# Performance work log

Hardware: AMD Instinct MI355X
Metric: run time of the kernel (lower is better)

Reference implementation:

```python
import jax, jax.numpy as jnp
import numpy as np

B, T, H, P, N = 32, 512, 128, 16, 16
D = 4 * H


def _lstm(x, Wih, Whh, bih, bhh):
    # standard torch-style LSTM, batch_first input x: [B, T, 1], zero init state
    Bz = x.shape[0]
    Hh = Whh.shape[1]
    h0 = jnp.zeros((Bz, Hh), x.dtype)

    def step(carry, xt):
        h, c = carry
        g = xt @ Wih.T + bih + h @ Whh.T + bhh  # [B, 4H], gate order i,f,g,o
        i, f, gg, o = jnp.split(g, 4, axis=-1)
        c = jax.nn.sigmoid(f) * c + jax.nn.sigmoid(i) * jnp.tanh(gg)
        h = jax.nn.sigmoid(o) * jnp.tanh(c)
        return (h, c), h

    _, hs = jax.lax.scan(step, (h0, h0), jnp.swapaxes(x, 0, 1))
    return jnp.swapaxes(hs, 0, 1)  # [B, T, H]


def _forward(Y, Xp, Xn, Xi, init_c, init_h, Wih, Whh, bih, bhh,
             Wc, Uc, bc, Wg, Ug, bg, Wf, Uf, bf, Wo, Uo, bo, Wa,
             Watt, batt, vatt, W1, b1, W2, b2, W3, b3):
    run = lambda x: _lstm(x, Wih, Whh, bih, bhh)
    Y1 = run(Y)                                              # [B,T,H]
    Xi1 = run(Xi)
    Xp1 = jnp.mean(jax.vmap(run)(jnp.moveaxis(Xp, 1, 0)), axis=0)  # mean over P stocks
    Xn1 = jnp.mean(jax.vmap(run)(jnp.moveaxis(Xn, 1, 0)), axis=0)
    result = jnp.concatenate([Y1, Xp1, Xn1, Xi1], axis=2)    # [B,T,4H]

    Hh = Wa.shape[0]

    def mi_step(carry, xt):  # Mi-LSTM cell: 4 input streams with gated-candidate attention
        c, h = carry
        xs = xt.reshape(xt.shape[0], 4, Hh)                  # split 4H into 4 streams
        cand = jnp.tanh(jnp.einsum('bkh,khj->bkj', xs, Wc) + jnp.einsum('bh,khj->bkj', h, Uc) + bc)
        ig = jax.nn.sigmoid(jnp.einsum('bkh,khj->bkj', xs, Wg) + jnp.einsum('bh,khj->bkj', h, Ug) + bg)
        l = ig * cand                                        # [B,4,H]
        a = jax.nn.softmax(jnp.einsum('bkj,bj->bk', l, c @ Wa), axis=1)
        lmix = jnp.einsum('bk,bkj->bj', a, l)
        f = jax.nn.sigmoid(xt @ Wf + h @ Uf + bf)
        o = jax.nn.sigmoid(xt @ Wo + h @ Uo + bo)
        c = f * c + lmix
        h = o * jnp.tanh(c)
        return (c, h), h

    _, hs = jax.lax.scan(mi_step, (init_c, init_h), jnp.swapaxes(result, 0, 1))
    Y2 = jnp.swapaxes(hs, 0, 1)                              # [B,T,H]

    # temporal attention over the Mi-LSTM outputs
    scores = jnp.tanh(Y2 @ Watt + batt) @ vatt               # [B,T]
    attw = jax.nn.softmax(scores, axis=1)
    Y3 = jnp.einsum('bt,bth->bh', attw, Y2)                  # [B,H]

    hm = jax.nn.relu(Y3 @ W1 + b1)
    hm = jax.nn.relu(hm @ W2 + b2)
    return hm @ W3 + b3                                      # [B,1]


def setup_inputs() -> dict:
    key = jax.random.key(0)
    ks = jax.random.split(key, 24)
    u = lambda k, s: jax.random.uniform(k, s, dtype=jnp.float32)
    nr = lambda k, s: jax.random.normal(k, s, dtype=jnp.float32) * 0.05
    z = lambda s: jnp.zeros(s, jnp.float32)
    return {
        'Y': u(ks[0], (B, T, 1)), 'Xp': u(ks[1], (B, P, T, 1)), 'Xn': u(ks[2], (B, N, T, 1)),
        'Xi': u(ks[3], (B, T, 1)), 'Target': u(ks[4], (B, 1)),
        'init_c': u(ks[5], (B, H)), 'init_h': u(ks[6], (B, H)),
        'Wih': nr(ks[7], (4 * H, 1)), 'Whh': nr(ks[8], (4 * H, H)), 'bih': z(4 * H), 'bhh': z(4 * H),
        'Wc': nr(ks[9], (4, H, H)), 'Uc': nr(ks[10], (4, H, H)), 'bc': z((4, H)),
        'Wg': nr(ks[11], (4, H, H)), 'Ug': nr(ks[12], (4, H, H)), 'bg': z((4, H)),
        'Wf': nr(ks[13], (D, H)), 'Uf': nr(ks[14], (H, H)), 'bf': z(H),
        'Wo': nr(ks[15], (D, H)), 'Uo': nr(ks[16], (H, H)), 'bo': z(H),
        'Wa': nr(ks[17], (H, H)),
        'Watt': nr(ks[18], (H, H)), 'batt': z(H), 'vatt': nr(ks[19], (H,)),
        'W1': nr(ks[20], (H, H)), 'b1': z(H),
        'W2': nr(ks[21], (H, H)), 'b2': z(H),
        'W3': nr(ks[22], (H, 1)), 'b3': z(1),
    }


def reference(Y, Xp, Xn, Xi, Target, init_c, init_h, Wih, Whh, bih, bhh,
              Wc, Uc, bc, Wg, Ug, bg, Wf, Uf, bf, Wo, Uo, bo, Wa,
              Watt, batt, vatt, W1, b1, W2, b2, W3, b3):
    out = _forward(Y, Xp, Xn, Xi, init_c, init_h, Wih, Whh, bih, bhh,
                   Wc, Uc, bc, Wg, Ug, bg, Wf, Uf, bf, Wo, Uo, bo, Wa,
                   Watt, batt, vatt, W1, b1, W2, b2, W3, b3)
    loss = jnp.mean((out - Target) ** 2)
    return out, loss
```

## Files before the change

### kernel.cpp

```cpp
#include <hip/hip_runtime.h>
#include <hip/hip_fp16.h>

typedef _Float16 half8 __attribute__((ext_vector_type(8)));
typedef float float4_ __attribute__((ext_vector_type(4)));

__device__ __forceinline__ float rcp_(float x) { return __builtin_amdgcn_rcpf(x); }
__device__ __forceinline__ float sigf(float x) { return rcp_(1.f + __expf(-x)); }
__device__ __forceinline__ float tanhf2(float x) {
  x = fminf(fmaxf(x, -15.f), 15.f);
  float e = __expf(-2.f * x);
  return (1.f - e) * rcp_(1.f + e);
}

__global__ __launch_bounds__(512, 2)
void k1_lstm(const float* __restrict__ Y, const float* __restrict__ Xp,
             const float* __restrict__ Xn, const float* __restrict__ Xi,
             const float* __restrict__ Wih, const float* __restrict__ Whh,
             const float* __restrict__ bih, const float* __restrict__ bhh,
             _Float16* __restrict__ result)
{
  __shared__ float x_lds[16][513];
  __shared__ _Float16 hbuf[2][16][136];

  const int tid  = threadIdx.x;
  const int wv   = tid >> 6;
  const int lane = tid & 63;
  const int cl   = lane & 15;
  const int rowg = lane >> 4;
  const int bid  = blockIdx.x;

  const float* xsrc; int slot; int do_mean; int b_out_base;
  if (bid < 2)       { xsrc = Y  + (size_t)(bid * 16) * 512;        slot = 0; do_mean = 0; b_out_base = bid * 16; }
  else if (bid < 4)  { xsrc = Xi + (size_t)((bid - 2) * 16) * 512;  slot = 3; do_mean = 0; b_out_base = (bid - 2) * 16; }
  else if (bid < 36) { xsrc = Xp + (size_t)((bid - 4) * 16) * 512;  slot = 1; do_mean = 1; b_out_base = bid - 4; }
  else               { xsrc = Xn + (size_t)((bid - 36) * 16) * 512; slot = 2; do_mean = 1; b_out_base = bid - 36; }

  for (int i = tid; i < 16 * 512; i += 512) {
    int r = i >> 9, t = i & 511;
    x_lds[r][t] = xsrc[r * 512 + t];
  }
  for (int i = tid; i < 16 * 136; i += 512) {
    hbuf[0][i / 136][i % 136] = (_Float16)0.f;
  }

  const int cg = wv * 16 + cl;
  half8 bw[4][4];
  #pragma unroll
  for (int g = 0; g < 4; ++g) {
    #pragma unroll
    for (int kc = 0; kc < 4; ++kc) {
      const float* p = Whh + (size_t)(g * 128 + cg) * 128 + kc * 32 + rowg * 8;
      half8 v;
      #pragma unroll
      for (int j = 0; j < 8; ++j) v[j] = (_Float16)p[j];
      bw[g][kc] = v;
    }
  }
  float wih_r[4], bias_r[4];
  #pragma unroll
  for (int g = 0; g < 4; ++g) {
    wih_r[g]  = Wih[g * 128 + cg];
    bias_r[g] = bih[g * 128 + cg] + bhh[g * 128 + cg];
  }

  float c_reg[4] = {0.f, 0.f, 0.f, 0.f};
  float hvp[4] = {0.f, 0.f, 0.f, 0.f};
  float sprev = 0.f;
  __syncthreads();

  for (int t = 0; t < 512; ++t) {
    if (t > 0) {
      if (!do_mean) {
        #pragma unroll
        for (int i = 0; i < 4; ++i) {
          int b = b_out_base + rowg * 4 + i;
          result[(((size_t)b * 512 + (t - 1)) * 4 + slot) * 128 + cg] = (_Float16)hvp[i];
        }
      } else {
        if (rowg == 0)
          result[(((size_t)b_out_base * 512 + (t - 1)) * 4 + slot) * 128 + cg] = (_Float16)sprev;
      }
    }

    const int cur = t & 1;
    half8 a[4];
    #pragma unroll
    for (int kc = 0; kc < 4; ++kc)
      a[kc] = *(const half8*)&hbuf[cur][cl][kc * 32 + rowg * 8];

    float4_ acc[4];
    #pragma unroll
    for (int g = 0; g < 4; ++g) {
      float4_ z = {0.f, 0.f, 0.f, 0.f};
      #pragma unroll
      for (int kc = 0; kc < 4; ++kc)
        z = __builtin_amdgcn_mfma_f32_16x16x32_f16(a[kc], bw[g][kc], z, 0, 0, 0);
      acc[g] = z;
    }

    float hv[4];
    #pragma unroll
    for (int i = 0; i < 4; ++i) {
      const int row = rowg * 4 + i;
      float x  = x_lds[row][t];
      float ui = acc[0][i] + x * wih_r[0] + bias_r[0];
      float uf = acc[1][i] + x * wih_r[1] + bias_r[1];
      float ug = acc[2][i] + x * wih_r[2] + bias_r[2];
      float uo = acc[3][i] + x * wih_r[3] + bias_r[3];
      float ii = sigf(ui), ff = sigf(uf), gg = tanhf2(ug), oo = sigf(uo);
      float c  = ff * c_reg[i] + ii * gg;
      c_reg[i] = c;
      float h  = oo * tanhf2(c);
      hv[i] = h;
      hbuf[cur ^ 1][row][cg] = (_Float16)h;
    }

    if (!do_mean) {
      #pragma unroll
      for (int i = 0; i < 4; ++i) hvp[i] = hv[i];
    } else {
      float s = hv[0] + hv[1] + hv[2] + hv[3];
      s += __shfl_xor(s, 16, 64);
      s += __shfl_xor(s, 32, 64);
      sprev = s * 0.0625f;
    }
    __syncthreads();
  }

  if (!do_mean) {
    #pragma unroll
    for (int i = 0; i < 4; ++i) {
      int b = b_out_base + rowg * 4 + i;
      result[(((size_t)b * 512 + 511) * 4 + slot) * 128 + cg] = (_Float16)hvp[i];
    }
  } else {
    if (rowg == 0)
      result[(((size_t)b_out_base * 512 + 511) * 4 + slot) * 128 + cg] = (_Float16)sprev;
  }
}

__global__ __launch_bounds__(512, 2)
void k2_gemm(const _Float16* __restrict__ result,
             const float* __restrict__ Wc, const float* __restrict__ Wg,
             const float* __restrict__ Wf, const float* __restrict__ Wo,
             _Float16* __restrict__ candX, _Float16* __restrict__ igX,
             _Float16* __restrict__ fX, _Float16* __restrict__ oX)
{
  __shared__ _Float16 a_lds[128][136];
  __shared__ _Float16 bt_lds[256][136];

  const int tid   = threadIdx.x;
  const int lane  = tid & 63;
  const int wv    = tid >> 6;
  const int cl    = lane & 15, rowg = lane >> 4;
  const int mtile = blockIdx.x;
  const int role  = blockIdx.y;

  const int nchunks = (role == 0) ? 4 : 1;
  const int kstream = role - 1;

  float4_ acc[16];
  #pragma unroll
  for (int n = 0; n < 16; ++n) acc[n] = (float4_){0.f, 0.f, 0.f, 0.f};

  for (int ch = 0; ch < nchunks; ++ch) {
    const int koff = (role == 0) ? ch * 128 : kstream * 128;
    for (int i = tid; i < 1024; i += 512) {
      int r = i >> 3, v8 = i & 7;
      half8 val = *(const half8*)&result[((size_t)(mtile * 128 + r)) * 512 + koff + v8 * 8];
      *(half8*)&a_lds[r][v8 * 8] = val;
    }
    for (int i = tid; i < 128 * 256; i += 512) {
      int n = i & 255, kk = i >> 8;
      float w;
      if (role == 0) {
        w = (n < 128) ? Wf[(size_t)(ch * 128 + kk) * 128 + n]
                      : Wo[(size_t)(ch * 128 + kk) * 128 + (n - 128)];
      } else {
        w = (n < 128) ? Wc[(size_t)(kstream * 128 + kk) * 128 + n]
                      : Wg[(size_t)(kstream * 128 + kk) * 128 + (n - 128)];
      }
      bt_lds[n][kk] = (_Float16)w;
    }
    __syncthreads();
    #pragma unroll
    for (int kc = 0; kc < 4; ++kc) {
      half8 a = *(const half8*)&a_lds[wv * 16 + cl][kc * 32 + rowg * 8];
      #pragma unroll
      for (int n = 0; n < 16; ++n) {
        half8 bb = *(const half8*)&bt_lds[n * 16 + cl][kc * 32 + rowg * 8];
        acc[n] = __builtin_amdgcn_mfma_f32_16x16x32_f16(a, bb, acc[n], 0, 0, 0);
      }
    }
    __syncthreads();
  }

  #pragma unroll
  for (int n = 0; n < 16; ++n) {
    int col = n * 16 + cl;
    #pragma unroll
    for (int i = 0; i < 4; ++i) {
      size_t r = (size_t)mtile * 128 + wv * 16 + rowg * 4 + i;
      _Float16 v = (_Float16)acc[n][i];
      if (role == 0) {
        if (col < 128) fX[r * 128 + col] = v;
        else           oX[r * 128 + (col - 128)] = v;
      } else {
        if (col < 128) candX[(r * 4 + kstream) * 128 + col] = v;
        else           igX  [(r * 4 + kstream) * 128 + (col - 128)] = v;
      }
    }
  }
}

__global__ __launch_bounds__(512, 1)
void k3_scan(const float* __restrict__ Uc, const float* __restrict__ Ug,
             const float* __restrict__ Uf, const float* __restrict__ Uo,
             const float* __restrict__ Wa,
             const float* __restrict__ bc, const float* __restrict__ bg,
             const float* __restrict__ bfv, const float* __restrict__ bov,
             const float* __restrict__ init_c, const float* __restrict__ init_h,
             const _Float16* __restrict__ candX, const _Float16* __restrict__ igX,
             const _Float16* __restrict__ fX, const _Float16* __restrict__ oX,
             _Float16* __restrict__ Y2)
{
  __shared__ __align__(16) unsigned h_pk[64];
  __shared__ __align__(16) unsigned c_pk[64];
  __shared__ float c_f32[128];
  __shared__ __align__(16) float raw[1408];
  __shared__ float part2[2][4];

  const int tid  = threadIdx.x;
  const int b    = blockIdx.x;
  const int wv   = tid >> 6;
  const int lane = tid & 63;
  const int cl   = lane & 15;
  const int rowg = lane >> 4;

  half8 wfrag[11][4];
  #pragma unroll
  for (int gi = 0; gi < 11; ++gi) {
    const int col = (wv * 11 + gi) * 16 + cl;
    const float* src;
    if (col < 512)       src = Uc + (col >> 7) * 16384 + (col & 127);
    else if (col < 1024) src = Ug + ((col >> 7) - 4) * 16384 + (col & 127);
    else if (col < 1152) src = Uf + (col - 1024);
    else if (col < 1280) src = Uo + (col - 1152);
    else                 src = Wa + (col - 1280);
    #pragma unroll
    for (int kc = 0; kc < 4; ++kc) {
      half8 v;
      #pragma unroll
      for (int j = 0; j < 8; ++j)
        v[j] = (_Float16)src[(kc * 32 + rowg * 8 + j) * 128];
      wfrag[gi][kc] = v;
    }
  }

  float bc_r[4] = {0, 0, 0, 0}, bg_r[4] = {0, 0, 0, 0}, bf_r = 0.f, bo_r = 0.f;
  if (tid < 128) {
    #pragma unroll
    for (int k = 0; k < 4; ++k) { bc_r[k] = bc[k * 128 + tid]; bg_r[k] = bg[k * 128 + tid]; }
    bf_r = bfv[tid]; bo_r = bov[tid];
    c_f32[tid] = init_c[b * 128 + tid];
  }
  if (tid < 64) {
    union { _Float16 h[2]; unsigned u; } hp, cp;
    hp.h[0] = (_Float16)init_h[b * 128 + 2 * tid];
    hp.h[1] = (_Float16)init_h[b * 128 + 2 * tid + 1];
    cp.h[0] = (_Float16)init_c[b * 128 + 2 * tid];
    cp.h[1] = (_Float16)init_c[b * 128 + 2 * tid + 1];
    h_pk[tid] = hp.u;
    c_pk[tid] = cp.u;
  }
  __syncthreads();

  float hprev = 0.f;

  for (int t = 0; t < 512; ++t) {
    if (t > 0 && tid < 128)
      Y2[((size_t)b * 512 + (t - 1)) * 128 + tid] = (_Float16)hprev;

    float cx[4] = {0, 0, 0, 0}, gx[4] = {0, 0, 0, 0}, fx = 0.f, ox = 0.f;
    if (tid < 128) {
      size_t r = (size_t)b * 512 + t;
      #pragma unroll
      for (int k = 0; k < 4; ++k) {
        cx[k] = (float)candX[(r * 4 + k) * 128 + tid];
        gx[k] = (float)igX  [(r * 4 + k) * 128 + tid];
      }
      fx = (float)fX[r * 128 + tid];
      ox = (float)oX[r * 128 + tid];
    }

    {
      const uint4* hp4 = (const uint4*)h_pk;
      const uint4* cp4 = (const uint4*)c_pk;
      union { uint4 u; half8 h; } hb[4], cb[4];
      #pragma unroll
      for (int kc = 0; kc < 4; ++kc) {
        hb[kc].u = hp4[kc * 4 + rowg];
        cb[kc].u = cp4[kc * 4 + rowg];
      }
      #pragma unroll
      for (int gi = 0; gi < 11; ++gi) {
        const int g = wv * 11 + gi;
        float4_ acc = {0.f, 0.f, 0.f, 0.f};
        if (g < 80) {
          #pragma unroll
          for (int kc = 0; kc < 4; ++kc)
            acc = __builtin_amdgcn_mfma_f32_16x16x32_f16(wfrag[gi][kc], hb[kc].h, acc, 0, 0, 0);
        } else {
          #pragma unroll
          for (int kc = 0; kc < 4; ++kc)
            acc = __builtin_amdgcn_mfma_f32_16x16x32_f16(wfrag[gi][kc], cb[kc].h, acc, 0, 0, 0);
        }
        if (cl == 0)
          *(float4_*)&raw[g * 16 + rowg * 4] = acc;
      }
    }
    __syncthreads();

    float l0 = 0.f, l1 = 0.f, l2 = 0.f, l3 = 0.f, fj = 0.f, oj = 0.f;
    if (tid < 128) {
      float cand[4], ig[4];
      #pragma unroll
      for (int k = 0; k < 4; ++k) {
        float uc = cx[k] + raw[k * 128 + tid] + bc_r[k];
        float ui = gx[k] + raw[512 + k * 128 + tid] + bg_r[k];
        cand[k] = tanhf2(uc);
        ig[k]   = sigf(ui);
      }
      l0 = ig[0] * cand[0]; l1 = ig[1] * cand[1];
      l2 = ig[2] * cand[2]; l3 = ig[3] * cand[3];
      float cwa = raw[1280 + tid];
      float p0 = l0 * cwa, p1 = l1 * cwa, p2 = l2 * cwa, p3 = l3 * cwa;
      #pragma unroll
      for (int m = 1; m < 64; m <<= 1) {
        p0 += __shfl_xor(p0, m, 64);
        p1 += __shfl_xor(p1, m, 64);
        p2 += __shfl_xor(p2, m, 64);
        p3 += __shfl_xor(p3, m, 64);
      }
      if ((tid & 63) == 0) {
        part2[tid >> 6][0] = p0; part2[tid >> 6][1] = p1;
        part2[tid >> 6][2] = p2; part2[tid >> 6][3] = p3;
      }
      fj = sigf(fx + raw[1024 + tid] + bf_r);
      oj = sigf(ox + raw[1152 + tid] + bo_r);
    }
    __syncthreads();

    if (tid < 128) {
      float d0 = part2[0][0] + part2[1][0];
      float d1 = part2[0][1] + part2[1][1];
      float d2 = part2[0][2] + part2[1][2];
      float d3 = part2[0][3] + part2[1][3];
      float mx = fmaxf(fmaxf(d0, d1), fmaxf(d2, d3));
      float e0 = __expf(d0 - mx), e1 = __expf(d1 - mx);
      float e2 = __expf(d2 - mx), e3 = __expf(d3 - mx);
      float inv = rcp_(e0 + e1 + e2 + e3);
      float lmix = (e0 * l0 + e1 * l1 + e2 * l2 + e3 * l3) * inv;
      float c = fj * c_f32[tid] + lmix;
      c_f32[tid] = c;
      float h = oj * tanhf2(c);
      ((_Float16*)h_pk)[tid] = (_Float16)h;
      ((_Float16*)c_pk)[tid] = (_Float16)c;
      hprev = h;
    }
    __syncthreads();
  }

  if (tid < 128)
    Y2[((size_t)b * 512 + 511) * 128 + tid] = (_Float16)hprev;
}

__global__ __launch_bounds__(256, 1)
void k4_attn(const _Float16* __restrict__ Y2,
             const float* __restrict__ Watt, const float* __restrict__ batt,
             const float* __restrict__ vatt,
             const float* __restrict__ W1, const float* __restrict__ b1,
             const float* __restrict__ W2, const float* __restrict__ b2,
             const float* __restrict__ W3, const float* __restrict__ b3,
             float* __restrict__ out)
{
  __shared__ _Float16 wt_lds[128][136];
  __shared__ float sc[512];
  __shared__ float red[8];
  __shared__ float y3[128];
  __shared__ float hm[128];

  const int tid = threadIdx.x;
  const int b   = blockIdx.x;
  const int lane = tid & 63, wv = tid >> 6;
  const int cl = lane & 15, rowg = lane >> 4;

  for (int i = tid; i < 128 * 128; i += 256) {
    int h = i >> 7, j = i & 127;
    wt_lds[j][h] = (_Float16)Watt[h * 128 + j];
  }
  __syncthreads();

  half8 bw[8][4];
  #pragma unroll
  for (int n = 0; n < 8; ++n)
    #pragma unroll
    for (int kc = 0; kc < 4; ++kc)
      bw[n][kc] = *(const half8*)&wt_lds[n * 16 + cl][kc * 32 + rowg * 8];
  float battr[8], vattr[8];
  #pragma unroll
  for (int n = 0; n < 8; ++n) { battr[n] = batt[n * 16 + cl]; vattr[n] = vatt[n * 16 + cl]; }

  for (int mt = wv * 8; mt < wv * 8 + 8; ++mt) {
    half8 a[4];
    #pragma unroll
    for (int kc = 0; kc < 4; ++kc)
      a[kc] = *(const half8*)&Y2[((size_t)b * 512 + mt * 16 + cl) * 128 + kc * 32 + rowg * 8];
    float sp[4] = {0.f, 0.f, 0.f, 0.f};
    #pragma unroll
    for (int n = 0; n < 8; ++n) {
      float4_ acc = {0.f, 0.f, 0.f, 0.f};
      #pragma unroll
      for (int kc = 0; kc < 4; ++kc)
        acc = __builtin_amdgcn_mfma_f32_16x16x32_f16(a[kc], bw[n][kc], acc, 0, 0, 0);
      #pragma unroll
      for (int i = 0; i < 4; ++i)
        sp[i] += tanhf2(acc[i] + battr[n]) * vattr[n];
    }
    #pragma unroll
    for (int i = 0; i < 4; ++i) {
      #pragma unroll
      for (int m = 1; m < 16; m <<= 1) sp[i] += __shfl_xor(sp[i], m, 64);
    }
    if (cl == 0) {
      #pragma unroll
      for (int i = 0; i < 4; ++i) sc[mt * 16 + rowg * 4 + i] = sp[i];
    }
  }
  __syncthreads();

  float v0 = sc[tid], v1 = sc[tid + 256];
  float mx = fmaxf(v0, v1);
  #pragma unroll
  for (int m = 1; m < 64; m <<= 1) mx = fmaxf(mx, __shfl_xor(mx, m, 64));
  if (lane == 0) red[wv] = mx;
  __syncthreads();
  mx = fmaxf(fmaxf(red[0], red[1]), fmaxf(red[2], red[3]));
  float e0 = __expf(v0 - mx), e1 = __expf(v1 - mx);
  float s = e0 + e1;
  #pragma unroll
  for (int m = 1; m < 64; m <<= 1) s += __shfl_xor(s, m, 64);
  __syncthreads();
  if (lane == 0) red[wv] = s;
  __syncthreads();
  float inv = rcp_(red[0] + red[1] + red[2] + red[3]);
  sc[tid] = e0 * inv;
  sc[tid + 256] = e1 * inv;
  __syncthreads();

  {
    int h = tid & 127, part = tid >> 7;
    float acc = 0.f;
    for (int t = part * 256; t < part * 256 + 256; ++t)
      acc += sc[t] * (float)Y2[((size_t)b * 512 + t) * 128 + h];
    if (part == 0) y3[h] = acc;
    __syncthreads();
    if (part == 1) y3[h] += acc;
    __syncthreads();
  }

  if (tid < 128) {
    float a1 = 0.f;
    for (int h2 = 0; h2 < 128; ++h2) a1 += y3[h2] * W1[h2 * 128 + tid];
    hm[tid] = fmaxf(a1 + b1[tid], 0.f);
  }
  __syncthreads();
  if (tid < 128) {
    float a2 = 0.f;
    for (int h2 = 0; h2 < 128; ++h2) a2 += hm[h2] * W2[h2 * 128 + tid];
    a2 = fmaxf(a2 + b2[tid], 0.f);
    float p = a2 * W3[tid];
    #pragma unroll
    for (int m = 1; m < 64; m <<= 1) p += __shfl_xor(p, m, 64);
    if ((tid & 63) == 0) red[4 + (tid >> 6)] = p;
  }
  __syncthreads();
  if (tid == 0) out[b] = red[4] + red[5] + b3[0];
}

__global__ void k5_loss(const float* __restrict__ out, const float* __restrict__ target,
                        float* __restrict__ loss_out)
{
  int l = threadIdx.x;
  float v = 0.f;
  if (l < 32) { float d = out[l] - target[l]; v = d * d; }
  #pragma unroll
  for (int m = 1; m < 64; m <<= 1) v += __shfl_xor(v, m, 64);
  if (l == 0) loss_out[0] = v * (1.f / 32.f);
}

extern "C" void kernel_launch(void* const* d_in, const int* in_sizes, int n_in,
                              void* d_out, int out_size, void* d_ws, size_t ws_size,
                              hipStream_t stream)
{
  const float* Y      = (const float*)d_in[0];
  const float* Xp     = (const float*)d_in[1];
  const float* Xn     = (const float*)d_in[2];
  const float* Xi     = (const float*)d_in[3];
  const float* Target = (const float*)d_in[4];
  const float* init_c = (const float*)d_in[5];
  const float* init_h = (const float*)d_in[6];
  const float* Wih    = (const float*)d_in[7];
  const float* Whh    = (const float*)d_in[8];
  const float* bih    = (const float*)d_in[9];
  const float* bhh    = (const float*)d_in[10];
  const float* Wc     = (const float*)d_in[11];
  const float* Uc     = (const float*)d_in[12];
  const float* bc     = (const float*)d_in[13];
  const float* Wg     = (const float*)d_in[14];
  const float* Ug     = (const float*)d_in[15];
  const float* bg     = (const float*)d_in[16];
  const float* Wf     = (const float*)d_in[17];
  const float* Uf     = (const float*)d_in[18];
  const float* bf     = (const float*)d_in[19];
  const float* Wo     = (const float*)d_in[20];
  const float* Uo     = (const float*)d_in[21];
  const float* bo     = (const float*)d_in[22];
  const float* Wa     = (const float*)d_in[23];
  const float* Watt   = (const float*)d_in[24];
  const float* batt   = (const float*)d_in[25];
  const float* vatt   = (const float*)d_in[26];
  const float* W1     = (const float*)d_in[27];
  const float* b1     = (const float*)d_in[28];
  const float* W2     = (const float*)d_in[29];
  const float* b2     = (const float*)d_in[30];
  const float* W3     = (const float*)d_in[31];
  const float* b3     = (const float*)d_in[32];

  char* ws = (char*)d_ws;
  _Float16* result = (_Float16*)(ws);
  _Float16* candX  = (_Float16*)(ws + ((size_t)16 << 20));
  _Float16* igX    = (_Float16*)(ws + ((size_t)32 << 20));
  _Float16* fXp    = (_Float16*)(ws + ((size_t)48 << 20));
  _Float16* oXp    = (_Float16*)(ws + ((size_t)52 << 20));
  _Float16* Y2     = (_Float16*)(ws + ((size_t)56 << 20));
  float* outp = (float*)d_out;

  k1_lstm<<<dim3(68), dim3(512), 0, stream>>>(Y, Xp, Xn, Xi, Wih, Whh, bih, bhh, result);
  k2_gemm<<<dim3(128, 5), dim3(512), 0, stream>>>(result, Wc, Wg, Wf, Wo, candX, igX, fXp, oXp);
  k3_scan<<<dim3(32), dim3(512), 0, stream>>>(Uc, Ug, Uf, Uo, Wa, bc, bg, bf, bo,
                                              init_c, init_h, candX, igX, fXp, oXp, Y2);
  k4_attn<<<dim3(32), dim3(256), 0, stream>>>(Y2, Watt, batt, vatt, W1, b1, W2, b2, W3, b3, outp);
  k5_loss<<<dim3(1), dim3(64), 0, stream>>>(outp, Target, outp + 32);
}
```

Baseline: 1.850 ms.

## Stage Mi-LSTM scan inputs and outputs in LDS per 16-step chunk

The 512-step recurrent scan is split into 32 chunks of 16 steps. At the start of each chunk, all 512 threads cooperatively load that chunk's precomputed candX/igX/fX/oX slices into shared memory with 16-byte vector loads, and every step then reads its inputs from LDS instead of issuing scattered global loads. The hidden outputs are likewise buffered in LDS and written to Y2 once per chunk as coalesced uint4 stores rather than once per step. This takes global memory latency off the serial per-step path, at the cost of about 40KB more LDS and an extra barrier-bound bulk load at each chunk boundary.

```diff
diff --git a/kernel.cpp b/kernel.cpp
--- a/kernel.cpp
+++ b/kernel.cpp
@@ -229,6 +229,11 @@
   __shared__ float c_f32[128];
   __shared__ __align__(16) float raw[1408];
   __shared__ float part2[2][4];
+  __shared__ __align__(16) _Float16 in_c[16 * 512];
+  __shared__ __align__(16) _Float16 in_g[16 * 512];
+  __shared__ __align__(16) _Float16 in_f[16 * 128];
+  __shared__ __align__(16) _Float16 in_o[16 * 128];
+  __shared__ __align__(16) _Float16 y2s[16 * 128];
 
   const int tid  = threadIdx.x;
   const int b    = blockIdx.x;
@@ -275,104 +280,118 @@
   }
   __syncthreads();
 
-  float hprev = 0.f;
-
-  for (int t = 0; t < 512; ++t) {
-    if (t > 0 && tid < 128)
-      Y2[((size_t)b * 512 + (t - 1)) * 128 + tid] = (_Float16)hprev;
-
-    float cx[4] = {0, 0, 0, 0}, gx[4] = {0, 0, 0, 0}, fx = 0.f, ox = 0.f;
-    if (tid < 128) {
-      size_t r = (size_t)b * 512 + t;
-      #pragma unroll
-      for (int k = 0; k < 4; ++k) {
-        cx[k] = (float)candX[(r * 4 + k) * 128 + tid];
-        gx[k] = (float)igX  [(r * 4 + k) * 128 + tid];
-      }
-      fx = (float)fX[r * 128 + tid];
-      ox = (float)oX[r * 128 + tid];
-    }
-
+  uint4* y2g = (uint4*)Y2;
+
+  for (int chunk = 0; chunk < 32; ++chunk) {
+    if (chunk > 0 && tid < 256)
+      y2g[(size_t)b * 8192 + (size_t)(chunk - 1) * 256 + tid] = ((const uint4*)y2s)[tid];
     {
-      const uint4* hp4 = (const uint4*)h_pk;
-      const uint4* cp4 = (const uint4*)c_pk;
-      union { uint4 u; half8 h; } hb[4], cb[4];
-      #pragma unroll
-      for (int kc = 0; kc < 4; ++kc) {
-        hb[kc].u = hp4[kc * 4 + rowg];
-        cb[kc].u = cp4[kc * 4 + rowg];
-      }
-      #pragma unroll
-      for (int gi = 0; gi < 11; ++gi) {
-        const int g = wv * 11 + gi;
-        float4_ acc = {0.f, 0.f, 0.f, 0.f};
-        if (g < 80) {
-          #pragma unroll
-          for (int kc = 0; kc < 4; ++kc)
-            acc = __builtin_amdgcn_mfma_f32_16x16x32_f16(wfrag[gi][kc], hb[kc].h, acc, 0, 0, 0);
-        } else {
-          #pragma unroll
-          for (int kc = 0; kc < 4; ++kc)
-            acc = __builtin_amdgcn_mfma_f32_16x16x32_f16(wfrag[gi][kc], cb[kc].h, acc, 0, 0, 0);
-        }
-        if (cl == 0)
-          *(float4_*)&raw[g * 16 + rowg * 4] = acc;
-      }
+      const uint4* c4 = (const uint4*)(candX + ((size_t)b * 512 + chunk * 16) * 512);
+      const uint4* g4 = (const uint4*)(igX   + ((size_t)b * 512 + chunk * 16) * 512);
+      ((uint4*)in_c)[tid]       = c4[tid];
+      ((uint4*)in_c)[tid + 512] = c4[tid + 512];
+      ((uint4*)in_g)[tid]       = g4[tid];
+      ((uint4*)in_g)[tid + 512] = g4[tid + 512];
+      if (tid < 256)
+        ((uint4*)in_f)[tid] = ((const uint4*)(fX + ((size_t)b * 512 + chunk * 16) * 128))[tid];
+      else
+        ((uint4*)in_o)[tid - 256] = ((const uint4*)(oX + ((size_t)b * 512 + chunk * 16) * 128))[tid - 256];
     }
     __syncthreads();
 
-    float l0 = 0.f, l1 = 0.f, l2 = 0.f, l3 = 0.f, fj = 0.f, oj = 0.f;
-    if (tid < 128) {
-      float cand[4], ig[4];
-      #pragma unroll
-      for (int k = 0; k < 4; ++k) {
-        float uc = cx[k] + raw[k * 128 + tid] + bc_r[k];
-        float ui = gx[k] + raw[512 + k * 128 + tid] + bg_r[k];
-        cand[k] = tanhf2(uc);
-        ig[k]   = sigf(ui);
-      }
-      l0 = ig[0] * cand[0]; l1 = ig[1] * cand[1];
-      l2 = ig[2] * cand[2]; l3 = ig[3] * cand[3];
-      float cwa = raw[1280 + tid];
-      float p0 = l0 * cwa, p1 = l1 * cwa, p2 = l2 * cwa, p3 = l3 * cwa;
-      #pragma unroll
-      for (int m = 1; m < 64; m <<= 1) {
-        p0 += __shfl_xor(p0, m, 64);
-        p1 += __shfl_xor(p1, m, 64);
-        p2 += __shfl_xor(p2, m, 64);
-        p3 += __shfl_xor(p3, m, 64);
-      }
-      if ((tid & 63) == 0) {
-        part2[tid >> 6][0] = p0; part2[tid >> 6][1] = p1;
-        part2[tid >> 6][2] = p2; part2[tid >> 6][3] = p3;
-      }
-      fj = sigf(fx + raw[1024 + tid] + bf_r);
-      oj = sigf(ox + raw[1152 + tid] + bo_r);
-    }
-    __syncthreads();
-
-    if (tid < 128) {
-      float d0 = part2[0][0] + part2[1][0];
-      float d1 = part2[0][1] + part2[1][1];
-      float d2 = part2[0][2] + part2[1][2];
-      float d3 = part2[0][3] + part2[1][3];
-      float mx = fmaxf(fmaxf(d0, d1), fmaxf(d2, d3));
-      float e0 = __expf(d0 - mx), e1 = __expf(d1 - mx);
-      float e2 = __expf(d2 - mx), e3 = __expf(d3 - mx);
-      float inv = rcp_(e0 + e1 + e2 + e3);
-      float lmix = (e0 * l0 + e1 * l1 + e2 * l2 + e3 * l3) * inv;
-      float c = fj * c_f32[tid] + lmix;
-      c_f32[tid] = c;
-      float h = oj * tanhf2(c);
-      ((_Float16*)h_pk)[tid] = (_Float16)h;
-      ((_Float16*)c_pk)[tid] = (_Float16)c;
-      hprev = h;
-    }
-    __syncthreads();
-  }
-
-  if (tid < 128)
-    Y2[((size_t)b * 512 + 511) * 128 + tid] = (_Float16)hprev;
+    for (int s = 0; s < 16; ++s) {
+      float cx[4] = {0, 0, 0, 0}, gx[4] = {0, 0, 0, 0}, fx = 0.f, ox = 0.f;
+      if (tid < 128) {
+        #pragma unroll
+        for (int k = 0; k < 4; ++k) {
+          cx[k] = (float)in_c[(s * 4 + k) * 128 + tid];
+          gx[k] = (float)in_g[(s * 4 + k) * 128 + tid];
+        }
+        fx = (float)in_f[s * 128 + tid];
+        ox = (float)in_o[s * 128 + tid];
+      }
+
+      {
+        const uint4* hp4 = (const uint4*)h_pk;
+        const uint4* cp4 = (const uint4*)c_pk;
+        union { uint4 u; half8 h; } hb[4], cb[4];
+        #pragma unroll
+        for (int kc = 0; kc < 4; ++kc) {
+          hb[kc].u = hp4[kc * 4 + rowg];
+          cb[kc].u = cp4[kc * 4 + rowg];
+        }
+        #pragma unroll
+        for (int gi = 0; gi < 11; ++gi) {
+          const int g = wv * 11 + gi;
+          float4_ acc = {0.f, 0.f, 0.f, 0.f};
+          if (g < 80) {
+            #pragma unroll
+            for (int kc = 0; kc < 4; ++kc)
+              acc = __builtin_amdgcn_mfma_f32_16x16x32_f16(wfrag[gi][kc], hb[kc].h, acc, 0, 0, 0);
+          } else {
+            #pragma unroll
+            for (int kc = 0; kc < 4; ++kc)
+              acc = __builtin_amdgcn_mfma_f32_16x16x32_f16(wfrag[gi][kc], cb[kc].h, acc, 0, 0, 0);
+          }
+          if (cl == 0)
+            *(float4_*)&raw[g * 16 + rowg * 4] = acc;
+        }
+      }
+      __syncthreads();
+
+      float l0 = 0.f, l1 = 0.f, l2 = 0.f, l3 = 0.f, fj = 0.f, oj = 0.f;
+      if (tid < 128) {
+        float cand[4], ig[4];
+        #pragma unroll
+        for (int k = 0; k < 4; ++k) {
+          float uc = cx[k] + raw[k * 128 + tid] + bc_r[k];
+          float ui = gx[k] + raw[512 + k * 128 + tid] + bg_r[k];
+          cand[k] = tanhf2(uc);
+          ig[k]   = sigf(ui);
+        }
+        l0 = ig[0] * cand[0]; l1 = ig[1] * cand[1];
+        l2 = ig[2] * cand[2]; l3 = ig[3] * cand[3];
+        float cwa = raw[1280 + tid];
+        float p0 = l0 * cwa, p1 = l1 * cwa, p2 = l2 * cwa, p3 = l3 * cwa;
+        #pragma unroll
+        for (int m = 1; m < 64; m <<= 1) {
+          p0 += __shfl_xor(p0, m, 64);
+          p1 += __shfl_xor(p1, m, 64);
+          p2 += __shfl_xor(p2, m, 64);
+          p3 += __shfl_xor(p3, m, 64);
+        }
+        if ((tid & 63) == 0) {
+          part2[tid >> 6][0] = p0; part2[tid >> 6][1] = p1;
+          part2[tid >> 6][2] = p2; part2[tid >> 6][3] = p3;
+        }
+        fj = sigf(fx + raw[1024 + tid] + bf_r);
+        oj = sigf(ox + raw[1152 + tid] + bo_r);
+      }
+      __syncthreads();
+
+      if (tid < 128) {
+        float d0 = part2[0][0] + part2[1][0];
+        float d1 = part2[0][1] + part2[1][1];
+        float d2 = part2[0][2] + part2[1][2];
+        float d3 = part2[0][3] + part2[1][3];
+        float mx = fmaxf(fmaxf(d0, d1), fmaxf(d2, d3));
+        float e0 = __expf(d0 - mx), e1 = __expf(d1 - mx);
+        float e2 = __expf(d2 - mx), e3 = __expf(d3 - mx);
+        float inv = rcp_(e0 + e1 + e2 + e3);
+        float lmix = (e0 * l0 + e1 * l1 + e2 * l2 + e3 * l3) * inv;
+        float c = fj * c_f32[tid] + lmix;
+        c_f32[tid] = c;
+        float h = oj * tanhf2(c);
+        ((_Float16*)h_pk)[tid] = (_Float16)h;
+        ((_Float16*)c_pk)[tid] = (_Float16)c;
+        y2s[s * 128 + tid] = (_Float16)h;
+      }
+      __syncthreads();
+    }
+  }
+
+  if (tid < 256)
+    y2g[(size_t)b * 8192 + (size_t)31 * 256 + tid] = ((const uint4*)y2s)[tid];
 }
 
 __global__ __launch_bounds__(256, 1)
```

Result: faster. 1.801 ms (-2.6%).
